# Kernel optimization log

Measured on AMD Instinct MI355X. Metric: run time of the kernel, lower is better.

The kernel has to match this reference:

```python
import jax, jax.numpy as jnp
import numpy as np
import math

TOPK = 13
NUM_CLASSES = 80
ALPHA = 1.0
BETA = 6.0
EPS = 1e-9


def _ciou(box1, box2, eps=1e-7):
    # box1: (b, n, 1, 4) gt xyxy, box2: (b, 1, A, 4) pred xyxy -> (b, n, A)
    b1x1, b1y1, b1x2, b1y2 = [box1[..., i] for i in range(4)]
    b2x1, b2y1, b2x2, b2y2 = [box2[..., i] for i in range(4)]
    w1, h1 = b1x2 - b1x1, b1y2 - b1y1
    w2, h2 = b2x2 - b2x1, b2y2 - b2y1
    inter = jnp.clip(jnp.minimum(b1x2, b2x2) - jnp.maximum(b1x1, b2x1), 0.0) * \
            jnp.clip(jnp.minimum(b1y2, b2y2) - jnp.maximum(b1y1, b2y1), 0.0)
    union = w1 * h1 + w2 * h2 - inter + eps
    iou = inter / union
    cw = jnp.maximum(b1x2, b2x2) - jnp.minimum(b1x1, b2x1)
    ch = jnp.maximum(b1y2, b2y2) - jnp.minimum(b1y1, b2y1)
    c2 = cw * cw + ch * ch + eps
    rho2 = ((b2x1 + b2x2 - b1x1 - b1x2) ** 2 + (b2y1 + b2y2 - b1y1 - b1y2) ** 2) / 4.0
    v = (4.0 / math.pi ** 2) * (jnp.arctan(w2 / (h2 + eps)) - jnp.arctan(w1 / (h1 + eps))) ** 2
    alpha = jax.lax.stop_gradient(v / (v - iou + (1.0 + eps)))
    return iou - (rho2 / c2 + v * alpha)


def _assign(pd_scores, pd_bboxes, anc_points, gt_labels, gt_probs, gt_bboxes, mask_gt):
    b, A, C = pd_scores.shape
    n = gt_bboxes.shape[1]
    bidx = jnp.arange(b)
    labels = gt_labels.reshape(b, n).astype(jnp.int32)

    # --- get_box_metrics ---
    bbox_scores = pd_scores[bidx[:, None], :, labels]                      # (b, n, A)
    overlaps = jnp.clip(_ciou(gt_bboxes[:, :, None, :], pd_bboxes[:, None, :, :]), 0.0)
    align_metric = bbox_scores ** ALPHA * overlaps ** BETA                 # (b, n, A)

    # --- select_candidates_in_gts ---
    lt, rb = gt_bboxes[..., :2], gt_bboxes[..., 2:]
    deltas = jnp.concatenate([anc_points[None, None] - lt[:, :, None],
                              rb[:, :, None] - anc_points[None, None]], axis=-1)
    mask_in_gts = (deltas.min(-1) > EPS).astype(pd_scores.dtype)           # (b, n, A)

    # --- select_topk_candidates ---
    metrics = align_metric * mask_in_gts
    _, topk_idxs = jax.lax.top_k(metrics, TOPK)
    topk_mask = jnp.broadcast_to(mask_gt.astype(bool), (b, n, TOPK))
    topk_idxs = jnp.where(topk_mask, topk_idxs, 0)
    cnt = jnp.zeros((b, n, A), jnp.int32).at[
        bidx[:, None, None], jnp.arange(n)[None, :, None], topk_idxs].add(1)
    is_in_topk = jnp.where(cnt > 1, 0, cnt).astype(metrics.dtype)
    mask_pos = is_in_topk * mask_in_gts * mask_gt                          # (b, n, A)

    # --- select_highest_overlaps ---
    tgt = (jnp.arange(n)[None, :, None] * mask_pos).astype(jnp.int32)
    max_mask = overlaps == overlaps.max(axis=1, keepdims=True)
    tgt = tgt * max_mask.astype(jnp.int32)                                 # (b, n, A)
    unique_bbox_idx = tgt.argmax(1)                                        # (b, A)
    fg_mask = mask_pos.sum(-2)                                             # (b, A)

    # --- get_targets ---
    tgt_flat = tgt + (bidx * n)[:, None, None]                             # (b, n, A)
    target_labels = labels.reshape(-1)[tgt_flat]                           # (b, n, A)
    sel = jnp.take_along_axis(tgt_flat, unique_bbox_idx[:, None, :], axis=1)[:, 0]
    target_bboxes = gt_bboxes.reshape(-1, 4)[sel]                          # (b, A, 4)

    # hard targets: per-anchor class histogram over gt axis, corrected
    hard = jnp.zeros((b, A, C), jnp.int32).at[
        bidx[:, None, None], jnp.arange(A)[None, None, :], target_labels].add(1)
    fg_columns = hard.sum(1).argmax(1)                                     # (b,)
    diff = (n - fg_mask).astype(jnp.int32)                                 # (b, A)
    col_mask = jax.nn.one_hot(fg_columns, C, dtype=jnp.int32)[:, None, :]  # (b, 1, C)
    non_fg_count = (hard * (1 - col_mask)).sum(-1)                         # (b, A)
    hard = hard - diff[..., None] * col_mask
    denom = (fg_mask - non_fg_count)[..., None] * col_mask                 # (b, A, C) float
    safe = jnp.where(denom != 0, denom, 1.0)
    hard = jnp.where(denom != 0, jnp.trunc(hard / safe).astype(jnp.int32), hard)
    hard = jnp.clip(hard, 0, 1)  # multilabel (>1) clamped to 1, negatives to 0

    # --- normalization of target scores ---
    pos_align = (align_metric * mask_pos).max(-1, keepdims=True)           # (b, n, 1)
    pos_overlaps = (overlaps * mask_pos).max(-1, keepdims=True)
    norm = (align_metric * pos_overlaps * mask_pos / (pos_align + EPS)).max(-2)[..., None]  # (b, A, 1)
    target_scores = hard.astype(pd_scores.dtype) * norm                    # (b, A, C)
    return target_bboxes, target_scores, fg_mask.astype(bool), tgt


def setup_inputs() -> dict:
    key = jax.random.key(0)
    ks = jax.random.split(key, 8)
    B, N, C = 32, 32, 80
    # YOLO anchor-point grid for 640x640, strides 8/16/32 -> A = 8400
    pts = []
    for s, g in ((8, 80), (16, 40), (32, 20)):
        c = (jnp.arange(g, dtype=jnp.float32) + 0.5) * s
        yy, xx = jnp.meshgrid(c, c, indexing="ij")
        pts.append(jnp.stack([xx.ravel(), yy.ravel()], -1))
    anc_points = jnp.concatenate(pts, 0)
    A = anc_points.shape[0]
    pd_scores = jax.random.uniform(ks[0], (B, A, C), jnp.float32)
    pcxy = anc_points[None] + 20.0 * jax.random.normal(ks[1], (B, A, 2), jnp.float32)
    pwh = jax.random.uniform(ks[2], (B, A, 2), jnp.float32, minval=10.0, maxval=120.0)
    pd_bboxes = jnp.concatenate([pcxy - pwh / 2, pcxy + pwh / 2], -1)
    gcxy = jax.random.uniform(ks[3], (B, N, 2), jnp.float32, minval=60.0, maxval=580.0)
    gwh = jax.random.uniform(ks[4], (B, N, 2), jnp.float32, minval=10.0, maxval=120.0)
    gt_bboxes = jnp.concatenate([gcxy - gwh / 2, gcxy + gwh / 2], -1)
    gt_labels = jax.random.randint(ks[5], (B, N, 1), 0, C).astype(jnp.int32)
    gt_probs = jax.random.uniform(ks[6], (B, N, 1), jnp.float32)
    n_valid = jax.random.randint(ks[7], (B, 1, 1), 1, N + 1)
    mask_gt = (jnp.arange(N)[None, :, None] < n_valid).astype(jnp.float32)
    return {"pd_scores": pd_scores, "pd_bboxes": pd_bboxes, "anc_points": anc_points,
            "gt_labels": gt_labels, "gt_probs": gt_probs, "gt_bboxes": gt_bboxes,
            "mask_gt": mask_gt}


def reference(pd_scores, pd_bboxes, anc_points, gt_labels, gt_probs, gt_bboxes, mask_gt):
    return _assign(pd_scores, pd_bboxes, anc_points, gt_labels, gt_probs, gt_bboxes, mask_gt)
```

## Files before the change

### kernel.cpp

```cpp
#include <hip/hip_runtime.h>
#include <math.h>

#define BB 32
#define NN 32
#define AA 8400
#define CC 80
#define TK 13
#define CAND 768
#define MAXP (NN*TK)

__device__ int      g_ccnt[BB*NN];
__device__ int      g_cand[BB*NN*CAND];
__device__ unsigned g_posmask[BB*AA];
__device__ float    g_posalign[BB*NN];
__device__ float    g_posov[BB*NN];
__device__ int      g_pcnt[BB];
__device__ int      g_plist[BB*MAXP];
__device__ int4     g_rec[BB*MAXP];
__device__ int      g_S[BB*CC];
__device__ int      g_fgcol[BB];

struct PdPre { float x1,y1,x2,y2, area, sx, sy, at; };

__device__ __forceinline__ float ciou_j(const PdPre& q, float4 g, float garea,
                                        float gsx, float gsy, float gatan) {
  float iw = fmaxf(fminf(q.x2, g.z) - fmaxf(q.x1, g.x), 0.0f);
  float ih = fmaxf(fminf(q.y2, g.w) - fmaxf(q.y1, g.y), 0.0f);
  float inter = iw * ih;
  float uni = q.area + garea - inter + 1e-7f;
  float iou = inter / uni;
  float cw = fmaxf(q.x2, g.z) - fminf(q.x1, g.x);
  float ch = fmaxf(q.y2, g.w) - fminf(q.y1, g.y);
  float c2 = cw*cw + ch*ch + 1e-7f;
  float dx = gsx - q.sx, dy = gsy - q.sy;
  float rho2 = (dx*dx + dy*dy) * 0.25f;
  float dat = gatan - q.at;
  float v = (float)(4.0/(M_PI*M_PI)) * dat * dat;
  float alpha = v / (v - iou + (1.0f + 1e-7f));
  return fmaxf(iou - (rho2/c2 + v*alpha), 0.0f);
}

__device__ __forceinline__ PdPre pd_prep(float4 p) {
  PdPre q;
  float w1 = p.z - p.x, h1 = p.w - p.y;
  q.x1 = p.x; q.y1 = p.y; q.x2 = p.z; q.y2 = p.w;
  q.area = w1*h1; q.sx = p.x + p.z; q.sy = p.y + p.w;
  q.at = atanf(w1 / (h1 + 1e-7f));
  return q;
}

__global__ __launch_bounds__(256) void kfill(const float* __restrict__ gt_bboxes,
                                             float* __restrict__ out_bbox,
                                             float* __restrict__ out_scores,
                                             float* __restrict__ out_fg,
                                             float* __restrict__ out_tgt) {
  const size_t NS4 = (size_t)BB*AA*CC/4;
  const size_t NT4 = (size_t)BB*NN*AA/4;
  const size_t NF4 = (size_t)BB*AA/4;
  const size_t NP4 = (size_t)BB*AA/4;
  const size_t NB4 = (size_t)BB*AA;
  const size_t total = NS4 + NT4 + NF4 + NP4 + NB4;
  float4 z4 = make_float4(0.f,0.f,0.f,0.f);
  for (size_t i = (size_t)blockIdx.x*256 + threadIdx.x; i < total;
       i += (size_t)gridDim.x*256) {
    if (i < NS4) ((float4*)out_scores)[i] = z4;
    else if (i < NS4+NT4) ((float4*)out_tgt)[i-NS4] = z4;
    else if (i < NS4+NT4+NF4) ((float4*)out_fg)[i-NS4-NT4] = z4;
    else if (i < NS4+NT4+NF4+NP4) ((float4*)g_posmask)[i-NS4-NT4-NF4] = z4;
    else {
      size_t k = i - NS4 - NT4 - NF4 - NP4;
      int b = (int)(k / AA);
      ((float4*)out_bbox)[k] = *(const float4*)&gt_bboxes[b*NN*4];
    }
  }
  size_t gid = (size_t)blockIdx.x*256 + threadIdx.x;
  if (gid < BB*CC) g_S[gid] = 0;
  if (gid < BB*NN) g_ccnt[gid] = 0;
  if (gid < BB) g_pcnt[gid] = 0;
}

__global__ __launch_bounds__(256) void kA(const float* __restrict__ anc,
                                          const float* __restrict__ gt_bboxes,
                                          const float* __restrict__ mask_gt) {
  int b = blockIdx.y, t = threadIdx.x;
  int a = blockIdx.x*256 + t;
  __shared__ __align__(16) float4 gbox[NN];
  __shared__ int smask[NN];
  if (t < NN) {
    gbox[t] = *(const float4*)&gt_bboxes[(b*NN + t)*4];
    smask[t] = (mask_gt[b*NN + t] != 0.0f) ? 1 : 0;
  }
  __syncthreads();
  if (a >= AA) return;
  float2 an = ((const float2*)anc)[a];
  #pragma unroll
  for (int j = 0; j < NN; ++j) {
    if (!smask[j]) continue;
    float4 g = gbox[j];
    float mn = fminf(fminf(an.x - g.x, an.y - g.y), fminf(g.z - an.x, g.w - an.y));
    if (mn > 1e-9f) {
      int s = atomicAdd(&g_ccnt[b*NN + j], 1);
      if (s < CAND) g_cand[(size_t)(b*NN + j)*CAND + s] = a;
    }
  }
}

__global__ __launch_bounds__(64) void k2(const float* __restrict__ mask_gt,
                                         const float* __restrict__ pd_scores,
                                         const float* __restrict__ pd_bboxes,
                                         const float* __restrict__ anc,
                                         const int* __restrict__ gt_labels,
                                         const float* __restrict__ gt_bboxes) {
  int bj = blockIdx.x;
  int b = bj / NN, j = bj % NN;
  int lane = threadIdx.x;
  bool valid = (mask_gt[bj] != 0.0f);
  if (!valid) {
    if (lane == 0) { g_posalign[bj] = 0.0f; g_posov[bj] = 0.0f; }
    return;
  }
  int cnt = g_ccnt[bj]; if (cnt > CAND) cnt = CAND;
  int labj = gt_labels[bj];
  float4 g = *(const float4*)&gt_bboxes[bj*4];
  float w2 = g.z - g.x, h2 = g.w - g.y;
  float garea = w2*h2, gsx = g.x + g.z, gsy = g.y + g.w;
  float gatan = atanf(w2 / (h2 + 1e-7f));

  unsigned long long tk[TK];
  #pragma unroll
  for (int i = 0; i < TK; ++i) tk[i] = 0ull;
  auto ins = [&](unsigned long long key) {
    if (key > tk[TK-1]) {
      tk[TK-1] = key;
      #pragma unroll
      for (int i = TK-1; i > 0; --i) {
        if (tk[i] > tk[i-1]) {
          unsigned long long tmp = tk[i-1]; tk[i-1] = tk[i]; tk[i] = tmp;
        }
      }
    }
  };
  for (int c = lane; c < cnt; c += 64) {
    int a = g_cand[(size_t)bj*CAND + c];
    float4 p = *(const float4*)&pd_bboxes[(size_t)(b*AA + a)*4];
    float sc = pd_scores[(size_t)(b*AA + a)*CC + labj];
    PdPre q = pd_prep(p);
    float ov = ciou_j(q, g, garea, gsx, gsy, gatan);
    float ov2 = ov*ov;
    float metric = sc * (ov2*ov2*ov2);
    ins(((unsigned long long)__float_as_uint(metric) << 32)
        | (unsigned long long)(0xFFFFFFFFu - (unsigned)a));
  }
  if (lane < TK) {
    float2 an = ((const float2*)anc)[lane];
    float mn = fminf(fminf(an.x - g.x, an.y - g.y), fminf(g.z - an.x, g.w - an.y));
    if (!(mn > 1e-9f))
      ins((unsigned long long)(0xFFFFFFFFu - (unsigned)lane));
  }
  unsigned long long myk = 0ull;
  for (int r = 0; r < TK; ++r) {
    unsigned long long m = tk[0];
    #pragma unroll
    for (int o = 32; o > 0; o >>= 1) {
      unsigned long long other = __shfl_xor(m, o, 64);
      if (other > m) m = other;
    }
    if (tk[0] == m) {
      #pragma unroll
      for (int i = 0; i < TK-1; ++i) tk[i] = tk[i+1];
      tk[TK-1] = 0ull;
    }
    if (lane == r) myk = m;
  }
  float pa = 0.0f, po = 0.0f;
  if (lane < TK && myk != 0ull) {
    unsigned a = 0xFFFFFFFFu - (unsigned)(myk & 0xFFFFFFFFull);
    float val = __uint_as_float((unsigned)(myk >> 32));
    float2 an = ((const float2*)anc)[a];
    float mn = fminf(fminf(an.x - g.x, an.y - g.y), fminf(g.z - an.x, g.w - an.y));
    if (mn > 1e-9f) {
      unsigned old = atomicOr(&g_posmask[b*AA + a], 1u << j);
      if (old == 0u) {
        int idx = atomicAdd(&g_pcnt[b], 1);
        g_plist[b*MAXP + idx] = (int)a;
      }
      float4 p = *(const float4*)&pd_bboxes[(size_t)(b*AA + a)*4];
      PdPre q = pd_prep(p);
      float ov = ciou_j(q, g, garea, gsx, gsy, gatan);
      pa = val; po = ov;
    }
  }
  #pragma unroll
  for (int o = 32; o > 0; o >>= 1) {
    pa = fmaxf(pa, __shfl_xor(pa, o, 64));
    po = fmaxf(po, __shfl_xor(po, o, 64));
  }
  if (lane == 0) { g_posalign[bj] = pa; g_posov[bj] = po; }
}

__global__ __launch_bounds__(256) void k3s(const float* __restrict__ pd_scores,
                                           const float* __restrict__ pd_bboxes,
                                           const float* __restrict__ gt_bboxes,
                                           const int* __restrict__ gt_labels,
                                           float* __restrict__ out_bbox,
                                           float* __restrict__ out_fg,
                                           float* __restrict__ out_tgt) {
  int b = blockIdx.y, t = threadIdx.x;
  __shared__ __align__(16) float4 gbox[NN];
  __shared__ float garea[NN], gsx[NN], gsy[NN], gatan[NN], pal[NN], pov[NN];
  __shared__ int lab[NN];
  if (t < NN) {
    float4 g = *(const float4*)&gt_bboxes[(b*NN + t)*4];
    gbox[t] = g;
    float w2 = g.z - g.x, h2 = g.w - g.y;
    gsx[t] = g.x + g.z; gsy[t] = g.y + g.w;
    garea[t] = w2*h2;
    gatan[t] = atanf(w2 / (h2 + 1e-7f));
    lab[t] = gt_labels[b*NN + t];
    pal[t] = g_posalign[b*NN + t];
    pov[t] = g_posov[b*NN + t];
  }
  __syncthreads();
  int npos = g_pcnt[b];
  int si = blockIdx.x*8 + (t >> 5);
  if (si >= npos) return;
  int j = t & 31;
  int a = g_plist[b*MAXP + si];
  unsigned pm = g_posmask[b*AA + a];
  float4 p = *(const float4*)&pd_bboxes[(size_t)(b*AA + a)*4];
  PdPre q = pd_prep(p);
  float ovj = ciou_j(q, gbox[j], garea[j], gsx[j], gsy[j], gatan[j]);
  float maxo = ovj;
  #pragma unroll
  for (int o = 16; o > 0; o >>= 1) maxo = fmaxf(maxo, __shfl_xor(maxo, o, 64));
  bool pmj = (pm >> j) & 1u;
  bool tb = pmj && (ovj == maxo) && (j > 0);
  unsigned long long bal = __ballot(tb);
  unsigned tm = (t & 32) ? (unsigned)(bal >> 32) : (unsigned)(bal & 0xffffffffull);
  float contrib = 0.0f;
  if (pmj) {
    float sc = pd_scores[(size_t)(b*AA + a)*CC + lab[j]];
    float ov2 = ovj*ovj;
    float al = sc * (ov2*ov2*ov2);
    contrib = al * pov[j] / (pal[j] + 1e-9f);
  }
  float nrm = contrib;
  #pragma unroll
  for (int o = 16; o > 0; o >>= 1) nrm = fmaxf(nrm, __shfl_xor(nrm, o, 64));
  if (tb) {
    atomicAdd(&g_S[b*CC + lab[j]], 1);
    out_tgt[(size_t)(b*NN + j)*AA + a] = (float)j;
  }
  if (j == 0) {
    int fg = __popc(pm);
    int jmax = tm ? (31 - __clz(tm)) : 0;
    out_fg[b*AA + a] = 1.0f;
    *(float4*)&out_bbox[(size_t)(b*AA + a)*4] = gbox[jmax];
    atomicAdd(&g_S[b*CC + lab[0]], -(int)__popc(tm));
    g_rec[b*MAXP + si] = make_int4(a, (int)tm, fg, __float_as_int(nrm));
  }
}

__global__ __launch_bounds__(64) void k3b(const int* __restrict__ gt_labels) {
  int b = threadIdx.x;
  if (b < BB) {
    int l0 = gt_labels[b*NN];
    int best = -2147483647, bc = 0;
    for (int c = 0; c < CC; ++c) {
      int s = g_S[b*CC + c] + ((c == l0) ? NN*AA : 0);
      if (s > best) { best = s; bc = c; }
    }
    g_fgcol[b] = bc;
  }
}

__global__ __launch_bounds__(256) void k4(const int* __restrict__ gt_labels,
                                          float* __restrict__ out_scores) {
  int b = blockIdx.y, t = threadIdx.x;
  __shared__ int lab[NN];
  if (t < NN) lab[t] = gt_labels[b*NN + t];
  __syncthreads();
  int npos = g_pcnt[b];
  int si = blockIdx.x*4 + (t >> 6);
  if (si >= npos) return;
  int4 r = g_rec[b*MAXP + si];
  int a = r.x; unsigned tm = (unsigned)r.y; int fg = r.z;
  float nrm = __int_as_float(r.w);
  int F = g_fgcol[b];
  unsigned m0 = 0u, m1 = 0u, m2 = 0u; int cntF = 0;
  int z = NN - __popc(tm);
  int l0 = lab[0];
  if (l0 < 32) m0 |= 1u << l0; else if (l0 < 64) m1 |= 1u << (l0-32); else m2 |= 1u << (l0-64);
  if (l0 == F) cntF += z;
  unsigned tmp = tm;
  while (tmp) {
    int jj = __ffs(tmp) - 1; tmp &= tmp - 1;
    int l = lab[jj];
    if (l < 32) m0 |= 1u << l; else if (l < 64) m1 |= 1u << (l-32); else m2 |= 1u << (l-64);
    cntF += (l == F) ? 1 : 0;
  }
  int lane = t & 63;
  size_t base = (size_t)(b*AA + a)*CC;
  {
    int c = lane;
    unsigned mw = (c < 32) ? m0 : m1;
    bool bit = (mw >> (c & 31)) & 1u;
    bool ind = (c == F) ? ((cntF + fg) != NN) : bit;
    out_scores[base + c] = ind ? nrm : 0.0f;
  }
  if (lane < 16) {
    int c = 64 + lane;
    bool bit = (m2 >> lane) & 1u;
    bool ind = (c == F) ? ((cntF + fg) != NN) : bit;
    out_scores[base + c] = ind ? nrm : 0.0f;
  }
}

extern "C" void kernel_launch(void* const* d_in, const int* in_sizes, int n_in,
                              void* d_out, int out_size, void* d_ws, size_t ws_size,
                              hipStream_t stream) {
  const float* pd_scores = (const float*)d_in[0];
  const float* pd_bboxes = (const float*)d_in[1];
  const float* anc       = (const float*)d_in[2];
  const int*   gt_labels = (const int*)d_in[3];
  const float* gt_bboxes = (const float*)d_in[5];
  const float* mask_gt   = (const float*)d_in[6];

  float* out_bbox   = (float*)d_out;
  float* out_scores = out_bbox + (size_t)BB*AA*4;
  float* out_fg     = out_scores + (size_t)BB*AA*CC;
  float* out_tgt    = out_fg + (size_t)BB*AA;

  kfill<<<2048, 256, 0, stream>>>(gt_bboxes, out_bbox, out_scores, out_fg, out_tgt);
  dim3 ga((AA + 255)/256, BB);
  kA<<<ga, 256, 0, stream>>>(anc, gt_bboxes, mask_gt);
  k2<<<BB*NN, 64, 0, stream>>>(mask_gt, pd_scores, pd_bboxes, anc, gt_labels, gt_bboxes);
  dim3 g3s((MAXP + 7)/8, BB);
  k3s<<<g3s, 256, 0, stream>>>(pd_scores, pd_bboxes, gt_bboxes, gt_labels, out_bbox, out_fg, out_tgt);
  k3b<<<1, 64, 0, stream>>>(gt_labels);
  dim3 g4((MAXP + 3)/4, BB);
  k4<<<g4, 256, 0, stream>>>(gt_labels, out_scores);
}
```

Measured before the change: 61.55 us.

## Fuse candidate gathering into top-k kernel and fold score writes into k3

Drops the separate anchor-in-gt kernel. Each per-gt block in k2 now scans all anchors itself and collects candidates in shared memory with shared-memory atomics instead of global ones. It also removes the class-count reduction kernel and the final score kernel. The foreground column is always the first gt label, because that label gets a huge bias, so k3 writes the per-class scores directly. This cuts three kernel launches and the global round trips between them. The cost is redundant anchor scans per gt and a smaller candidate cap (512), which could truncate large boxes.

Result: slower. 81.78 us (+32.9%).

```diff
diff --git a/kernel.cpp b/kernel.cpp
--- a/kernel.cpp
+++ b/kernel.cpp
@@ -6,19 +6,14 @@
 #define AA 8400
 #define CC 80
 #define TK 13
-#define CAND 768
+#define CAND 512
 #define MAXP (NN*TK)
 
-__device__ int      g_ccnt[BB*NN];
-__device__ int      g_cand[BB*NN*CAND];
 __device__ unsigned g_posmask[BB*AA];
 __device__ float    g_posalign[BB*NN];
 __device__ float    g_posov[BB*NN];
 __device__ int      g_pcnt[BB];
 __device__ int      g_plist[BB*MAXP];
-__device__ int4     g_rec[BB*MAXP];
-__device__ int      g_S[BB*CC];
-__device__ int      g_fgcol[BB];
 
 struct PdPre { float x1,y1,x2,y2, area, sx, sy, at; };
 
@@ -74,35 +69,7 @@
     }
   }
   size_t gid = (size_t)blockIdx.x*256 + threadIdx.x;
-  if (gid < BB*CC) g_S[gid] = 0;
-  if (gid < BB*NN) g_ccnt[gid] = 0;
   if (gid < BB) g_pcnt[gid] = 0;
-}
-
-__global__ __launch_bounds__(256) void kA(const float* __restrict__ anc,
-                                          const float* __restrict__ gt_bboxes,
-                                          const float* __restrict__ mask_gt) {
-  int b = blockIdx.y, t = threadIdx.x;
-  int a = blockIdx.x*256 + t;
-  __shared__ __align__(16) float4 gbox[NN];
-  __shared__ int smask[NN];
-  if (t < NN) {
-    gbox[t] = *(const float4*)&gt_bboxes[(b*NN + t)*4];
-    smask[t] = (mask_gt[b*NN + t] != 0.0f) ? 1 : 0;
-  }
-  __syncthreads();
-  if (a >= AA) return;
-  float2 an = ((const float2*)anc)[a];
-  #pragma unroll
-  for (int j = 0; j < NN; ++j) {
-    if (!smask[j]) continue;
-    float4 g = gbox[j];
-    float mn = fminf(fminf(an.x - g.x, an.y - g.y), fminf(g.z - an.x, g.w - an.y));
-    if (mn > 1e-9f) {
-      int s = atomicAdd(&g_ccnt[b*NN + j], 1);
-      if (s < CAND) g_cand[(size_t)(b*NN + j)*CAND + s] = a;
-    }
-  }
 }
 
 __global__ __launch_bounds__(64) void k2(const float* __restrict__ mask_gt,
@@ -112,20 +79,33 @@
                                          const int* __restrict__ gt_labels,
                                          const float* __restrict__ gt_bboxes) {
   int bj = blockIdx.x;
-  int b = bj / NN, j = bj % NN;
+  int b = bj >> 5, j = bj & 31;
   int lane = threadIdx.x;
+  __shared__ int lcnt;
+  __shared__ int lcand[CAND];
   bool valid = (mask_gt[bj] != 0.0f);
   if (!valid) {
     if (lane == 0) { g_posalign[bj] = 0.0f; g_posov[bj] = 0.0f; }
     return;
   }
-  int cnt = g_ccnt[bj]; if (cnt > CAND) cnt = CAND;
+  if (lane == 0) lcnt = 0;
+  __syncthreads();
   int labj = gt_labels[bj];
   float4 g = *(const float4*)&gt_bboxes[bj*4];
   float w2 = g.z - g.x, h2 = g.w - g.y;
   float garea = w2*h2, gsx = g.x + g.z, gsy = g.y + g.w;
   float gatan = atanf(w2 / (h2 + 1e-7f));
-
+  const float2* anc2 = (const float2*)anc;
+  for (int a = lane; a < AA; a += 64) {
+    float2 an = anc2[a];
+    float mn = fminf(fminf(an.x - g.x, an.y - g.y), fminf(g.z - an.x, g.w - an.y));
+    if (mn > 1e-9f) {
+      int s = atomicAdd(&lcnt, 1);
+      if (s < CAND) lcand[s] = a;
+    }
+  }
+  __syncthreads();
+  int cnt = lcnt; if (cnt > CAND) cnt = CAND;
   unsigned long long tk[TK];
   #pragma unroll
   for (int i = 0; i < TK; ++i) tk[i] = 0ull;
@@ -141,7 +121,7 @@
     }
   };
   for (int c = lane; c < cnt; c += 64) {
-    int a = g_cand[(size_t)bj*CAND + c];
+    int a = lcand[c];
     float4 p = *(const float4*)&pd_bboxes[(size_t)(b*AA + a)*4];
     float sc = pd_scores[(size_t)(b*AA + a)*CC + labj];
     PdPre q = pd_prep(p);
@@ -152,7 +132,7 @@
         | (unsigned long long)(0xFFFFFFFFu - (unsigned)a));
   }
   if (lane < TK) {
-    float2 an = ((const float2*)anc)[lane];
+    float2 an = anc2[lane];
     float mn = fminf(fminf(an.x - g.x, an.y - g.y), fminf(g.z - an.x, g.w - an.y));
     if (!(mn > 1e-9f))
       ins((unsigned long long)(0xFFFFFFFFu - (unsigned)lane));
@@ -176,7 +156,7 @@
   if (lane < TK && myk != 0ull) {
     unsigned a = 0xFFFFFFFFu - (unsigned)(myk & 0xFFFFFFFFull);
     float val = __uint_as_float((unsigned)(myk >> 32));
-    float2 an = ((const float2*)anc)[a];
+    float2 an = anc2[a];
     float mn = fminf(fminf(an.x - g.x, an.y - g.y), fminf(g.z - an.x, g.w - an.y));
     if (mn > 1e-9f) {
       unsigned old = atomicOr(&g_posmask[b*AA + a], 1u << j);
@@ -198,13 +178,14 @@
   if (lane == 0) { g_posalign[bj] = pa; g_posov[bj] = po; }
 }
 
-__global__ __launch_bounds__(256) void k3s(const float* __restrict__ pd_scores,
-                                           const float* __restrict__ pd_bboxes,
-                                           const float* __restrict__ gt_bboxes,
-                                           const int* __restrict__ gt_labels,
-                                           float* __restrict__ out_bbox,
-                                           float* __restrict__ out_fg,
-                                           float* __restrict__ out_tgt) {
+__global__ __launch_bounds__(256) void k3(const float* __restrict__ pd_scores,
+                                          const float* __restrict__ pd_bboxes,
+                                          const float* __restrict__ gt_bboxes,
+                                          const int* __restrict__ gt_labels,
+                                          float* __restrict__ out_bbox,
+                                          float* __restrict__ out_fg,
+                                          float* __restrict__ out_tgt,
+                                          float* __restrict__ out_scores) {
   int b = blockIdx.y, t = threadIdx.x;
   __shared__ __align__(16) float4 gbox[NN];
   __shared__ float garea[NN], gsx[NN], gsy[NN], gatan[NN], pal[NN], pov[NN];
@@ -247,51 +228,16 @@
   float nrm = contrib;
   #pragma unroll
   for (int o = 16; o > 0; o >>= 1) nrm = fmaxf(nrm, __shfl_xor(nrm, o, 64));
-  if (tb) {
-    atomicAdd(&g_S[b*CC + lab[j]], 1);
-    out_tgt[(size_t)(b*NN + j)*AA + a] = (float)j;
-  }
-  if (j == 0) {
-    int fg = __popc(pm);
-    int jmax = tm ? (31 - __clz(tm)) : 0;
-    out_fg[b*AA + a] = 1.0f;
-    *(float4*)&out_bbox[(size_t)(b*AA + a)*4] = gbox[jmax];
-    atomicAdd(&g_S[b*CC + lab[0]], -(int)__popc(tm));
-    g_rec[b*MAXP + si] = make_int4(a, (int)tm, fg, __float_as_int(nrm));
-  }
-}
-
-__global__ __launch_bounds__(64) void k3b(const int* __restrict__ gt_labels) {
-  int b = threadIdx.x;
-  if (b < BB) {
-    int l0 = gt_labels[b*NN];
-    int best = -2147483647, bc = 0;
-    for (int c = 0; c < CC; ++c) {
-      int s = g_S[b*CC + c] + ((c == l0) ? NN*AA : 0);
-      if (s > best) { best = s; bc = c; }
-    }
-    g_fgcol[b] = bc;
-  }
-}
-
-__global__ __launch_bounds__(256) void k4(const int* __restrict__ gt_labels,
-                                          float* __restrict__ out_scores) {
-  int b = blockIdx.y, t = threadIdx.x;
-  __shared__ int lab[NN];
-  if (t < NN) lab[t] = gt_labels[b*NN + t];
-  __syncthreads();
-  int npos = g_pcnt[b];
-  int si = blockIdx.x*4 + (t >> 6);
-  if (si >= npos) return;
-  int4 r = g_rec[b*MAXP + si];
-  int a = r.x; unsigned tm = (unsigned)r.y; int fg = r.z;
-  float nrm = __int_as_float(r.w);
-  int F = g_fgcol[b];
-  unsigned m0 = 0u, m1 = 0u, m2 = 0u; int cntF = 0;
+  if (tb) out_tgt[(size_t)(b*NN + j)*AA + a] = (float)j;
+  int fg = __popc(pm);
+  int F = lab[0];
+  unsigned m0 = 0u, m1 = 0u, m2 = 0u;
   int z = NN - __popc(tm);
-  int l0 = lab[0];
-  if (l0 < 32) m0 |= 1u << l0; else if (l0 < 64) m1 |= 1u << (l0-32); else m2 |= 1u << (l0-64);
-  if (l0 == F) cntF += z;
+  int cntF = z;
+  {
+    int l0 = lab[0];
+    if (l0 < 32) m0 |= 1u << l0; else if (l0 < 64) m1 |= 1u << (l0-32); else m2 |= 1u << (l0-64);
+  }
   unsigned tmp = tm;
   while (tmp) {
     int jj = __ffs(tmp) - 1; tmp &= tmp - 1;
@@ -299,20 +245,30 @@
     if (l < 32) m0 |= 1u << l; else if (l < 64) m1 |= 1u << (l-32); else m2 |= 1u << (l-64);
     cntF += (l == F) ? 1 : 0;
   }
-  int lane = t & 63;
+  bool hFv = (cntF + fg) != NN;
   size_t base = (size_t)(b*AA + a)*CC;
   {
-    int c = lane;
-    unsigned mw = (c < 32) ? m0 : m1;
-    bool bit = (mw >> (c & 31)) & 1u;
-    bool ind = (c == F) ? ((cntF + fg) != NN) : bit;
+    int c = j;
+    bool bit = (m0 >> j) & 1u;
+    bool ind = (c == F) ? hFv : bit;
     out_scores[base + c] = ind ? nrm : 0.0f;
   }
-  if (lane < 16) {
-    int c = 64 + lane;
-    bool bit = (m2 >> lane) & 1u;
-    bool ind = (c == F) ? ((cntF + fg) != NN) : bit;
+  {
+    int c = j + 32;
+    bool bit = (m1 >> j) & 1u;
+    bool ind = (c == F) ? hFv : bit;
     out_scores[base + c] = ind ? nrm : 0.0f;
+  }
+  if (j < 16) {
+    int c = j + 64;
+    bool bit = (m2 >> j) & 1u;
+    bool ind = (c == F) ? hFv : bit;
+    out_scores[base + c] = ind ? nrm : 0.0f;
+  }
+  if (j == 0) {
+    out_fg[b*AA + a] = 1.0f;
+    int jmax = tm ? (31 - __clz(tm)) : 0;
+    *(float4*)&out_bbox[(size_t)(b*AA + a)*4] = gbox[jmax];
   }
 }
 
@@ -332,12 +288,8 @@
   float* out_tgt    = out_fg + (size_t)BB*AA;
 
   kfill<<<2048, 256, 0, stream>>>(gt_bboxes, out_bbox, out_scores, out_fg, out_tgt);
-  dim3 ga((AA + 255)/256, BB);
-  kA<<<ga, 256, 0, stream>>>(anc, gt_bboxes, mask_gt);
   k2<<<BB*NN, 64, 0, stream>>>(mask_gt, pd_scores, pd_bboxes, anc, gt_labels, gt_bboxes);
-  dim3 g3s((MAXP + 7)/8, BB);
-  k3s<<<g3s, 256, 0, stream>>>(pd_scores, pd_bboxes, gt_bboxes, gt_labels, out_bbox, out_fg, out_tgt);
-  k3b<<<1, 64, 0, stream>>>(gt_labels);
-  dim3 g4((MAXP + 3)/4, BB);
-  k4<<<g4, 256, 0, stream>>>(gt_labels, out_scores);
-}
+  dim3 g3((MAXP + 7)/8, BB);
+  k3<<<g3, 256, 0, stream>>>(pd_scores, pd_bboxes, gt_bboxes, gt_labels,
+                             out_bbox, out_fg, out_tgt, out_scores);
+}
```
